# Kernel tuning notes

Measured on AMD Instinct MI355X. Metric: run time of the kernel, lower is better.

## Reference

```python
import jax, jax.numpy as jnp
import numpy as np

B, S, D_MODEL, H = 4, 2048, 1024, 16
DEPTH = D_MODEL // H  # 64


def setup_inputs() -> dict:
    key = jax.random.key(0)
    ks = jax.random.split(key, 12)
    inp = {
        "v": jax.random.normal(ks[0], (B, S, D_MODEL), jnp.float32),
        "k": jax.random.normal(ks[1], (B, S, D_MODEL), jnp.float32),
        "q": jax.random.normal(ks[2], (B, S, D_MODEL), jnp.float32),
        "mask": jnp.zeros((B, 1, 1, S), jnp.int32),  # unused by the layer
        # Dense(d_model) params (glorot-ish scale)
        "wq": jax.random.normal(ks[3], (D_MODEL, D_MODEL), jnp.float32) / np.sqrt(D_MODEL),
        "bq": jnp.zeros((D_MODEL,), jnp.float32),
        "wk": jax.random.normal(ks[4], (D_MODEL, D_MODEL), jnp.float32) / np.sqrt(D_MODEL),
        "bk": jnp.zeros((D_MODEL,), jnp.float32),
        "wv": jax.random.normal(ks[5], (D_MODEL, D_MODEL), jnp.float32) / np.sqrt(D_MODEL),
        "bv": jnp.zeros((D_MODEL,), jnp.float32),
        # global attention weights: [max_seq_len, 1], stddev=0.1
        "gqw": 0.1 * jax.random.normal(ks[6], (S, 1), jnp.float32),
        "gkw": 0.1 * jax.random.normal(ks[7], (S, 1), jnp.float32),
        "wo": jax.random.normal(ks[8], (D_MODEL, D_MODEL), jnp.float32) / np.sqrt(D_MODEL),
        "bo": jnp.zeros((D_MODEL,), jnp.float32),
    }
    return inp


def _split_heads(x):
    # [B, S, D] -> [B, H, S, depth]
    Bc = x.shape[0]
    return x.reshape(Bc, -1, H, DEPTH).transpose(0, 2, 1, 3)


def reference(v, k, q, mask, wq, bq, wk, bk, wv, bv, gqw, gkw, wo, bo):
    # QKV projections
    qh = _split_heads(q @ wq + bq)  # [B, H, S, depth]
    kh = _split_heads(k @ wk + bk)
    vh = _split_heads(v @ wv + bv)
    # Fastformer additive attention: mul -> seq-sum -> mul -> seq-sum -> mul -> add
    qh = qh * gqw                          # gqw [S,1] broadcasts over [B,H,S,depth]
    gq = jnp.sum(qh, axis=2, keepdims=True)  # global query [B,H,1,depth]
    kh = kh * gq * gkw
    gk = jnp.sum(kh, axis=2, keepdims=True)  # global key [B,H,1,depth]
    out = vh * gk + qh                       # [B,H,S,depth]
    # merge heads and output projection
    out = out.transpose(0, 2, 1, 3).reshape(out.shape[0], -1, D_MODEL)
    return out @ wo + bo
```

## Files before the change

kernel.cpp:

```cpp
#include <hip/hip_runtime.h>

#define DM 1024
#define BATCH 4
#define SEQ 2048
#define M_TOT (BATCH*SEQ)

typedef unsigned short ushort_t;
typedef __bf16 bf16x8 __attribute__((ext_vector_type(8)));
typedef float f32x4 __attribute__((ext_vector_type(4)));
typedef unsigned short u16x4 __attribute__((ext_vector_type(4)));
typedef unsigned short u16x8 __attribute__((ext_vector_type(8)));

__device__ __forceinline__ ushort_t f2bf(float f) {
  unsigned u = __builtin_bit_cast(unsigned, f);
  u = (u + 0x7fffu + ((u >> 16) & 1u)) >> 16;
  return (ushort_t)u;
}
__device__ __forceinline__ float bf2f(ushort_t h) {
  unsigned u = ((unsigned)h) << 16;
  return __builtin_bit_cast(float, u);
}

#define GLL(gp, lp)                                                            \
  __builtin_amdgcn_global_load_lds(                                            \
      (const __attribute__((address_space(1))) unsigned int*)(const void*)(gp),\
      (__attribute__((address_space(3))) unsigned int*)(void*)(lp), 16, 0, 0)

__device__ __forceinline__ size_t src_off(int row0, int e) {
  return (size_t)(row0 + (e >> 2)) * DM + (((e & 3) ^ ((e >> 3) & 3)) * 8);
}

__global__ void k_reduce(const float* __restrict__ q, const float* __restrict__ k,
                         const float* __restrict__ v,
                         const float* __restrict__ gqw, const float* __restrict__ gkw,
                         float* __restrict__ pq, float* __restrict__ pk,
                         float* __restrict__ G,
                         ushort_t* __restrict__ qb, ushort_t* __restrict__ vb) {
  const int b = blockIdx.x, sc = blockIdx.y;
  const int d0 = threadIdx.x * 4;
  const int s0 = sc * 8;
  const size_t base = ((size_t)b * SEQ + s0) * DM + d0;
  float aq0 = 0.f, aq1 = 0.f, aq2 = 0.f, aq3 = 0.f;
  float ak0 = 0.f, ak1 = 0.f, ak2 = 0.f, ak3 = 0.f;
  float sgq = 0.f, sgk = 0.f;
#pragma unroll
  for (int i = 0; i < 8; ++i) {
    const float wq_ = gqw[s0 + i], wk_ = gkw[s0 + i];
    const size_t off = base + (size_t)i * DM;
    const float4 qv = *(const float4*)(q + off);
    const float4 kv = *(const float4*)(k + off);
    const float4 vv = *(const float4*)(v + off);
    aq0 += wq_ * qv.x; aq1 += wq_ * qv.y; aq2 += wq_ * qv.z; aq3 += wq_ * qv.w;
    ak0 += wk_ * kv.x; ak1 += wk_ * kv.y; ak2 += wk_ * kv.z; ak3 += wk_ * kv.w;
    u16x4 oq, ov;
    oq[0] = f2bf(wq_ * qv.x); oq[1] = f2bf(wq_ * qv.y);
    oq[2] = f2bf(wq_ * qv.z); oq[3] = f2bf(wq_ * qv.w);
    ov[0] = f2bf(vv.x); ov[1] = f2bf(vv.y); ov[2] = f2bf(vv.z); ov[3] = f2bf(vv.w);
    *(u16x4*)(qb + off) = oq;
    *(u16x4*)(vb + off) = ov;
    sgq += wq_; sgk += wk_;
  }
  const size_t po = ((size_t)(sc * BATCH + b) << 10) + d0;
  *(float4*)(pq + po) = make_float4(aq0, aq1, aq2, aq3);
  *(float4*)(pk + po) = make_float4(ak0, ak1, ak2, ak3);
  if (b == 0 && threadIdx.x == 0) {
    atomicAdd(&G[0], sgq);
    atomicAdd(&G[1], sgk);
  }
}

__global__ void k_rsum(const float* __restrict__ pq, const float* __restrict__ pk,
                       float* __restrict__ qr, float* __restrict__ kr) {
  const int b = blockIdx.x;
  const int d = blockIdx.y * 256 + threadIdx.x;
  const int sg = blockIdx.z;
  float aq = 0.f, ak = 0.f;
#pragma unroll 4
  for (int s = sg * 32; s < sg * 32 + 32; ++s) {
    const size_t po = ((size_t)(s * BATCH + b) << 10) + d;
    aq += pq[po];
    ak += pk[po];
  }
  atomicAdd(&qr[b * DM + d], aq);
  atomicAdd(&kr[b * DM + d], ak);
}

__global__ void k_gpart(const float* __restrict__ wq, const float* __restrict__ wk,
                        const float* __restrict__ qr, const float* __restrict__ kr,
                        float* __restrict__ qacc, float* __restrict__ kacc) {
  const int d = blockIdx.x * 256 + threadIdx.x;
  const int k0 = blockIdx.y * 32;
  __shared__ float sq[4][32], sk[4][32];
  if (threadIdx.x < 128) {
    const int b = threadIdx.x >> 5, kk = threadIdx.x & 31;
    sq[b][kk] = qr[b * DM + k0 + kk];
    sk[b][kk] = kr[b * DM + k0 + kk];
  }
  __syncthreads();
  float aq[4] = {0.f, 0.f, 0.f, 0.f}, ak[4] = {0.f, 0.f, 0.f, 0.f};
#pragma unroll 8
  for (int kk = 0; kk < 32; ++kk) {
    const float wqv = wq[(size_t)(k0 + kk) * DM + d];
    const float wkv = wk[(size_t)(k0 + kk) * DM + d];
#pragma unroll
    for (int b = 0; b < 4; ++b) {
      aq[b] += sq[b][kk] * wqv;
      ak[b] += sk[b][kk] * wkv;
    }
  }
#pragma unroll
  for (int b = 0; b < 4; ++b) {
    atomicAdd(&qacc[b * DM + d], aq[b]);
    atomicAdd(&kacc[b * DM + d], ak[b]);
  }
}

__global__ void k_gfin(const float* __restrict__ qacc, const float* __restrict__ kacc,
                       const float* __restrict__ bq, const float* __restrict__ bk,
                       const float* __restrict__ G, float* __restrict__ gk) {
  const int i = blockIdx.x * 256 + threadIdx.x;
  const int d = i & (DM - 1);
  const float gqv = qacc[i] + bq[d] * G[0];
  const float gkr = kacc[i] + bk[d] * G[1];
  gk[i] = gqv * gkr;
}

__global__ void k_conv(const float* __restrict__ x0, ushort_t* __restrict__ y0,
                       const float* __restrict__ x1, ushort_t* __restrict__ y1) {
  const float* x = blockIdx.y ? x1 : x0;
  ushort_t* y = blockIdx.y ? y1 : y0;
  size_t i = (size_t)blockIdx.x * 256 + threadIdx.x;
  const float4* p = (const float4*)x + i * 2;
  float4 a = p[0], b = p[1];
  u16x8 o;
  o[0] = f2bf(a.x); o[1] = f2bf(a.y); o[2] = f2bf(a.z); o[3] = f2bf(a.w);
  o[4] = f2bf(b.x); o[5] = f2bf(b.y); o[6] = f2bf(b.z); o[7] = f2bf(b.w);
  *(u16x8*)(y + i * 8) = o;
}

__global__ void k_trans(const float* __restrict__ W, ushort_t* __restrict__ T) {
  __shared__ float ls[32][33];
  const int bi = blockIdx.x, bj = blockIdx.y;
#pragma unroll
  for (int p = 0; p < 4; ++p) {
    int e = threadIdx.x + p * 256;
    int r = e >> 5, c = e & 31;
    ls[r][c] = W[(size_t)(bi * 32 + r) * DM + bj * 32 + c];
  }
  __syncthreads();
#pragma unroll
  for (int p = 0; p < 4; ++p) {
    int e = threadIdx.x + p * 256;
    int r = e >> 5, c = e & 31;
    T[(size_t)(bj * 32 + r) * DM + bi * 32 + c] = f2bf(ls[c][r]);
  }
}

__global__ void k_wog(const ushort_t* __restrict__ woT, const float* __restrict__ gk,
                      ushort_t* __restrict__ wogT) {
  const size_t i = (size_t)blockIdx.x * 256 + threadIdx.x;
  const size_t c = i * 8;
  const int j0 = (int)(c & (DM - 1));
  const int b = (int)(c >> 20);
  u16x8 wv = *(const u16x8*)(woT + (c & ((1u << 20) - 1)));
  const float4 g0 = *(const float4*)(gk + b * DM + j0);
  const float4 g1 = *(const float4*)(gk + b * DM + j0 + 4);
  float g[8] = {g0.x, g0.y, g0.z, g0.w, g1.x, g1.y, g1.z, g1.w};
  u16x8 o;
#pragma unroll
  for (int j = 0; j < 8; ++j) o[j] = f2bf(bf2f(wv[j]) * g[j]);
  *(u16x8*)(wogT + i * 8) = o;
}

__global__ void k_bias(const float* __restrict__ wo, const float* __restrict__ bq,
                       const float* __restrict__ bv, const float* __restrict__ gk,
                       float* __restrict__ qbias, float* __restrict__ vbias) {
  const int n = blockIdx.x * 256 + threadIdx.x;
  const int k0 = blockIdx.y * 32;
  float aq = 0.f, av[4] = {0.f, 0.f, 0.f, 0.f};
  for (int kk = 0; kk < 32; ++kk) {
    const float w = wo[(size_t)(k0 + kk) * DM + n];
    aq += bq[k0 + kk] * w;
    const float bw = bv[k0 + kk] * w;
#pragma unroll
    for (int b = 0; b < 4; ++b) av[b] += bw * gk[b * DM + k0 + kk];
  }
  atomicAdd(&qbias[n], aq);
#pragma unroll
  for (int b = 0; b < 4; ++b) atomicAdd(&vbias[b * DM + n], av[b]);
}

__global__ void k_small(const ushort_t* __restrict__ woT, const ushort_t* __restrict__ wogT,
                        const ushort_t* __restrict__ wqB, const ushort_t* __restrict__ wvB,
                        ushort_t* __restrict__ WqoT, ushort_t* __restrict__ WvbT) {
  __shared__ __align__(16) ushort_t lsA[3][128 * 32];
  __shared__ __align__(16) ushort_t lsB[3][128 * 32];
  const int z = blockIdx.z;
  const ushort_t* A  = z == 0 ? woT : wogT + (size_t)(z - 1) * (DM * DM);
  const ushort_t* Bt = z == 0 ? wqB : wvB;
  ushort_t* Out      = z == 0 ? WqoT : WvbT + (size_t)(z - 1) * (DM * DM);

  const int tid = threadIdx.x;
  const int w = tid >> 6, lane = tid & 63;
  const int m0 = blockIdx.x * 128, n0 = blockIdx.y * 128;
  const int wr = w >> 1, wc = w & 1;
  const int c0 = w * 2, c1 = c0 + 1;
  const int e0 = c0 * 64 + lane, e1 = c1 * 64 + lane;
  const ushort_t* gA0 = A + src_off(m0, e0);
  const ushort_t* gA1 = A + src_off(m0, e1);
  const ushort_t* gB0 = Bt + src_off(n0, e0);
  const ushort_t* gB1 = Bt + src_off(n0, e1);

  int aoff[4], boff[4];
#pragma unroll
  for (int i = 0; i < 4; ++i) {
    const int ra = wr * 64 + i * 16 + (lane & 15);
    aoff[i] = ra * 32 + (((lane >> 4) ^ ((ra >> 1) & 3)) * 8);
    const int rb = wc * 64 + i * 16 + (lane & 15);
    boff[i] = rb * 32 + (((lane >> 4) ^ ((rb >> 1) & 3)) * 8);
  }

  f32x4 acc[4][4];
#pragma unroll
  for (int i = 0; i < 4; ++i)
#pragma unroll
    for (int j = 0; j < 4; ++j) acc[i][j] = (f32x4){0.f, 0.f, 0.f, 0.f};

  auto STAGE = [&](int tt, int buf) {
    const int o = tt * 32;
    GLL(gA0 + o, &lsA[buf][c0 * 512]);
    GLL(gA1 + o, &lsA[buf][c1 * 512]);
    GLL(gB0 + o, &lsB[buf][c0 * 512]);
    GLL(gB1 + o, &lsB[buf][c1 * 512]);
  };

  STAGE(0, 0);
  STAGE(1, 1);
#pragma unroll 1
  for (int t = 0; t < 32; ++t) {
    if (t < 31) { asm volatile("s_waitcnt vmcnt(4)" ::: "memory"); }
    else        { asm volatile("s_waitcnt vmcnt(0)" ::: "memory"); }
    __builtin_amdgcn_s_barrier();
    if (t + 2 < 32) STAGE(t + 2, (t + 2) % 3);
    const int cur = t % 3;
    bf16x8 av[4], bv[4];
#pragma unroll
    for (int i = 0; i < 4; ++i) av[i] = *(const bf16x8*)(&lsA[cur][aoff[i]]);
#pragma unroll
    for (int j = 0; j < 4; ++j) bv[j] = *(const bf16x8*)(&lsB[cur][boff[j]]);
#pragma unroll
    for (int i = 0; i < 4; ++i)
#pragma unroll
      for (int j = 0; j < 4; ++j)
        acc[i][j] = __builtin_amdgcn_mfma_f32_16x16x32_bf16(av[i], bv[j], acc[i][j], 0, 0, 0);
  }

  const int lr = (lane >> 4) * 4, lc = lane & 15;
  const int rbase = m0 + wr * 64, cbase = n0 + wc * 64;
#pragma unroll
  for (int j = 0; j < 4; ++j) {
    const int col = cbase + j * 16 + lc;
#pragma unroll
    for (int i = 0; i < 4; ++i)
#pragma unroll
      for (int t = 0; t < 4; ++t)
        Out[(size_t)(rbase + i * 16 + lr + t) * DM + col] = f2bf(acc[i][j][t]);
  }
}

__global__ __launch_bounds__(512, 1)
void k_big(const ushort_t* __restrict__ qb, const ushort_t* __restrict__ vb,
           const ushort_t* __restrict__ WqoT, const ushort_t* __restrict__ WvbT,
           const float* __restrict__ gqw, const float* __restrict__ qbias,
           const float* __restrict__ vbias, const float* __restrict__ bo,
           float* __restrict__ Out) {
  __shared__ __align__(16) ushort_t lsA[3][256 * 64];
  __shared__ __align__(16) ushort_t lsB[3][128 * 64];
  const int tid = threadIdx.x;
  const int w = tid >> 6, lane = tid & 63;
  const int m0 = blockIdx.x * 256, n0 = blockIdx.y * 128;
  const int b = m0 >> 11;
  const int wr = w >> 2, wc = w & 3;

  const int subrow = lane >> 3;
  const int srcslot = (lane & 7) ^ subrow;
  size_t offA[4], offB[2];
#pragma unroll
  for (int p = 0; p < 4; ++p) {
    const int row = (4 * w + p) * 8 + subrow;
    offA[p] = (size_t)(m0 + row) * DM + srcslot * 8;
  }
#pragma unroll
  for (int p = 0; p < 2; ++p) {
    const int row = (2 * w + p) * 8 + subrow;
    offB[p] = (size_t)(n0 + row) * DM + srcslot * 8;
  }
  const ushort_t* Bv = WvbT + (size_t)b * (DM * DM);

  const int g = lane >> 4, l7 = lane & 7, l15 = lane & 15;
  int aoff[2][8], boff[2][2];
#pragma unroll
  for (int kh = 0; kh < 2; ++kh) {
#pragma unroll
    for (int i = 0; i < 8; ++i) {
      const int ra = wr * 128 + i * 16 + l15;
      aoff[kh][i] = ra * 64 + (((kh * 4 + g) ^ l7) * 8);
    }
#pragma unroll
    for (int j = 0; j < 2; ++j) {
      const int rb = wc * 32 + j * 16 + l15;
      boff[kh][j] = rb * 64 + (((kh * 4 + g) ^ l7) * 8);
    }
  }

  f32x4 acc[8][2];
#pragma unroll
  for (int i = 0; i < 8; ++i)
#pragma unroll
    for (int j = 0; j < 2; ++j) acc[i][j] = (f32x4){0.f, 0.f, 0.f, 0.f};

  auto SRC = [&](int tt, const ushort_t*& Ab, const ushort_t*& Bb, int& k0) {
    if (tt < 16) { Ab = qb; Bb = WqoT; k0 = tt * 64; }
    else         { Ab = vb; Bb = Bv;   k0 = (tt - 16) * 64; }
  };
  auto STAGE_H0 = [&](int tt, int buf) {
    const ushort_t *Ab, *Bb; int k0; SRC(tt, Ab, Bb, k0);
    GLL(Ab + offA[0] + k0, &lsA[buf][(4 * w + 0) * 512]);
    GLL(Ab + offA[1] + k0, &lsA[buf][(4 * w + 1) * 512]);
    GLL(Bb + offB[0] + k0, &lsB[buf][(2 * w + 0) * 512]);
  };
  auto STAGE_H1 = [&](int tt, int buf) {
    const ushort_t *Ab, *Bb; int k0; SRC(tt, Ab, Bb, k0);
    GLL(Ab + offA[2] + k0, &lsA[buf][(4 * w + 2) * 512]);
    GLL(Ab + offA[3] + k0, &lsA[buf][(4 * w + 3) * 512]);
    GLL(Bb + offB[1] + k0, &lsB[buf][(2 * w + 1) * 512]);
  };

  STAGE_H0(0, 0); STAGE_H1(0, 0);
  STAGE_H0(1, 1); STAGE_H1(1, 1);
#pragma unroll 1
  for (int t = 0; t < 32; ++t) {
    const int cur = t % 3, nb = (t + 2) % 3;
    const bool st = (t + 2 < 32);
    if (t < 31) { asm volatile("s_waitcnt vmcnt(6)\n\ts_barrier" ::: "memory"); }
    else        { asm volatile("s_waitcnt vmcnt(0)\n\ts_barrier" ::: "memory"); }
    {
      bf16x8 av[8], bv[2];
#pragma unroll
      for (int i = 0; i < 8; ++i) av[i] = *(const bf16x8*)(&lsA[cur][aoff[0][i]]);
#pragma unroll
      for (int j = 0; j < 2; ++j) bv[j] = *(const bf16x8*)(&lsB[cur][boff[0][j]]);
      if (st) STAGE_H0(t + 2, nb);
      __builtin_amdgcn_s_setprio(1);
#pragma unroll
      for (int i = 0; i < 8; ++i)
#pragma unroll
        for (int j = 0; j < 2; ++j)
          acc[i][j] = __builtin_amdgcn_mfma_f32_16x16x32_bf16(av[i], bv[j], acc[i][j], 0, 0, 0);
      __builtin_amdgcn_s_setprio(0);
      asm volatile("s_barrier" ::: "memory");
    }
    {
      bf16x8 av[8], bv[2];
#pragma unroll
      for (int i = 0; i < 8; ++i) av[i] = *(const bf16x8*)(&lsA[cur][aoff[1][i]]);
#pragma unroll
      for (int j = 0; j < 2; ++j) bv[j] = *(const bf16x8*)(&lsB[cur][boff[1][j]]);
      if (st) STAGE_H1(t + 2, nb);
      __builtin_amdgcn_s_setprio(1);
#pragma unroll
      for (int i = 0; i < 8; ++i)
#pragma unroll
        for (int j = 0; j < 2; ++j)
          acc[i][j] = __builtin_amdgcn_mfma_f32_16x16x32_bf16(av[i], bv[j], acc[i][j], 0, 0, 0);
      __builtin_amdgcn_s_setprio(0);
      asm volatile("s_barrier" ::: "memory");
    }
  }

  const int lr = (lane >> 4) * 4, lc = lane & 15;
  const int rbase = m0 + wr * 128, cbase = n0 + wc * 32;
#pragma unroll
  for (int j = 0; j < 2; ++j) {
    const int col = cbase + j * 16 + lc;
    const float qbn = qbias[col];
    const float cb = vbias[b * DM + col] + bo[col];
#pragma unroll
    for (int i = 0; i < 8; ++i)
#pragma unroll
      for (int r = 0; r < 4; ++r) {
        const int row = rbase + i * 16 + lr + r;
        Out[(size_t)row * DM + col] = acc[i][j][r] + gqw[row & (SEQ - 1)] * qbn + cb;
      }
  }
}

extern "C" void kernel_launch(void* const* d_in, const int* in_sizes, int n_in,
                              void* d_out, int out_size, void* d_ws, size_t ws_size,
                              hipStream_t stream) {
  const float* v   = (const float*)d_in[0];
  const float* k   = (const float*)d_in[1];
  const float* q   = (const float*)d_in[2];
  const float* wq  = (const float*)d_in[4];
  const float* bq  = (const float*)d_in[5];
  const float* wk  = (const float*)d_in[6];
  const float* bk  = (const float*)d_in[7];
  const float* wv  = (const float*)d_in[8];
  const float* bv  = (const float*)d_in[9];
  const float* gqw = (const float*)d_in[10];
  const float* gkw = (const float*)d_in[11];
  const float* wo  = (const float*)d_in[12];
  const float* bo  = (const float*)d_in[13];
  float* out = (float*)d_out;
  float* wsf = (float*)d_ws;

  float* qr    = wsf + 0;
  float* kr    = wsf + 4096;
  float* qacc  = wsf + 8192;
  float* kacc  = wsf + 12288;
  float* G     = wsf + 16384;
  float* qbias = wsf + 16640;
  float* vbias = wsf + 17664;
  float* gk    = wsf + 21760;
  ushort_t* b16  = (ushort_t*)((char*)d_ws + (1 << 17));
  ushort_t* qb   = b16;
  ushort_t* vb   = qb + (size_t)M_TOT * DM;
  ushort_t* wqB  = vb + (size_t)M_TOT * DM;
  ushort_t* wvB  = wqB + (size_t)DM * DM;
  ushort_t* woT  = wvB + (size_t)DM * DM;
  ushort_t* WqoT = woT + (size_t)DM * DM;
  ushort_t* WvbT = WqoT + (size_t)DM * DM;
  ushort_t* wogT = (ushort_t*)out;
  float* pq = out + (1 << 22);
  float* pk = pq + (1 << 20);

  hipMemsetAsync(d_ws, 0, 21760 * sizeof(float), stream);

  k_conv<<<dim3((DM * DM / 8) / 256, 2), 256, 0, stream>>>(wq, wqB, wv, wvB);
  k_trans<<<dim3(32, 32), 256, 0, stream>>>(wo, woT);

  k_reduce<<<dim3(BATCH, SEQ / 8), 256, 0, stream>>>(q, k, v, gqw, gkw, pq, pk, G, qb, vb);
  k_rsum<<<dim3(BATCH, DM / 256, 8), 256, 0, stream>>>(pq, pk, qr, kr);

  k_gpart<<<dim3(DM / 256, DM / 32), 256, 0, stream>>>(wq, wk, qr, kr, qacc, kacc);
  k_gfin<<<(BATCH * DM) / 256, 256, 0, stream>>>(qacc, kacc, bq, bk, G, gk);

  k_wog<<<(BATCH * DM * DM / 8) / 256, 256, 0, stream>>>(woT, gk, wogT);
  k_bias<<<dim3(DM / 256, DM / 32), 256, 0, stream>>>(wo, bq, bv, gk, qbias, vbias);

  k_small<<<dim3(8, 8, 5), 256, 0, stream>>>(woT, wogT, wqB, wvB, WqoT, WvbT);

  k_big<<<dim3(M_TOT / 256, DM / 128), 512, 0, stream>>>(
      qb, vb, WqoT, WvbT, gqw, qbias, vbias, bo, out);
}
```

Baseline: 127.5 us.

## Software-pipeline LDS fragment reads across MFMA halves and template GEMM for weight fold

The big GEMM loop is restructured so each half-tile's LDS fragment reads are issued before the previous half's MFMAs. This double-buffers register fragments and drops one barrier per half-step, so LDS latency hides behind matrix math. The separate small weight-product GEMM is replaced by a templated instance of the same pipelined kernel (256x128 tiles, 512 threads, fewer blocks). The cost is higher register pressure from the doubled fragments, and lower parallelism for the small GEMM with only 160 blocks.

Result: faster. 123.1 us (-3.4%).

```diff
diff --git a/kernel.cpp b/kernel.cpp
--- a/kernel.cpp
+++ b/kernel.cpp
@@ -25,10 +25,6 @@
   __builtin_amdgcn_global_load_lds(                                            \
       (const __attribute__((address_space(1))) unsigned int*)(const void*)(gp),\
       (__attribute__((address_space(3))) unsigned int*)(void*)(lp), 16, 0, 0)
-
-__device__ __forceinline__ size_t src_off(int row0, int e) {
-  return (size_t)(row0 + (e >> 2)) * DM + (((e & 3) ^ ((e >> 3) & 3)) * 8);
-}
 
 __global__ void k_reduce(const float* __restrict__ q, const float* __restrict__ k,
                          const float* __restrict__ v,
@@ -190,97 +186,29 @@
   for (int b = 0; b < 4; ++b) atomicAdd(&vbias[b * DM + n], av[b]);
 }
 
-__global__ void k_small(const ushort_t* __restrict__ woT, const ushort_t* __restrict__ wogT,
-                        const ushort_t* __restrict__ wqB, const ushort_t* __restrict__ wvB,
-                        ushort_t* __restrict__ WqoT, ushort_t* __restrict__ WvbT) {
-  __shared__ __align__(16) ushort_t lsA[3][128 * 32];
-  __shared__ __align__(16) ushort_t lsB[3][128 * 32];
-  const int z = blockIdx.z;
-  const ushort_t* A  = z == 0 ? woT : wogT + (size_t)(z - 1) * (DM * DM);
-  const ushort_t* Bt = z == 0 ? wqB : wvB;
-  ushort_t* Out      = z == 0 ? WqoT : WvbT + (size_t)(z - 1) * (DM * DM);
-
-  const int tid = threadIdx.x;
-  const int w = tid >> 6, lane = tid & 63;
-  const int m0 = blockIdx.x * 128, n0 = blockIdx.y * 128;
-  const int wr = w >> 1, wc = w & 1;
-  const int c0 = w * 2, c1 = c0 + 1;
-  const int e0 = c0 * 64 + lane, e1 = c1 * 64 + lane;
-  const ushort_t* gA0 = A + src_off(m0, e0);
-  const ushort_t* gA1 = A + src_off(m0, e1);
-  const ushort_t* gB0 = Bt + src_off(n0, e0);
-  const ushort_t* gB1 = Bt + src_off(n0, e1);
-
-  int aoff[4], boff[4];
-#pragma unroll
-  for (int i = 0; i < 4; ++i) {
-    const int ra = wr * 64 + i * 16 + (lane & 15);
-    aoff[i] = ra * 32 + (((lane >> 4) ^ ((ra >> 1) & 3)) * 8);
-    const int rb = wc * 64 + i * 16 + (lane & 15);
-    boff[i] = rb * 32 + (((lane >> 4) ^ ((rb >> 1) & 3)) * 8);
-  }
-
-  f32x4 acc[4][4];
-#pragma unroll
-  for (int i = 0; i < 4; ++i)
-#pragma unroll
-    for (int j = 0; j < 4; ++j) acc[i][j] = (f32x4){0.f, 0.f, 0.f, 0.f};
-
-  auto STAGE = [&](int tt, int buf) {
-    const int o = tt * 32;
-    GLL(gA0 + o, &lsA[buf][c0 * 512]);
-    GLL(gA1 + o, &lsA[buf][c1 * 512]);
-    GLL(gB0 + o, &lsB[buf][c0 * 512]);
-    GLL(gB1 + o, &lsB[buf][c1 * 512]);
-  };
-
-  STAGE(0, 0);
-  STAGE(1, 1);
-#pragma unroll 1
-  for (int t = 0; t < 32; ++t) {
-    if (t < 31) { asm volatile("s_waitcnt vmcnt(4)" ::: "memory"); }
-    else        { asm volatile("s_waitcnt vmcnt(0)" ::: "memory"); }
-    __builtin_amdgcn_s_barrier();
-    if (t + 2 < 32) STAGE(t + 2, (t + 2) % 3);
-    const int cur = t % 3;
-    bf16x8 av[4], bv[4];
-#pragma unroll
-    for (int i = 0; i < 4; ++i) av[i] = *(const bf16x8*)(&lsA[cur][aoff[i]]);
-#pragma unroll
-    for (int j = 0; j < 4; ++j) bv[j] = *(const bf16x8*)(&lsB[cur][boff[j]]);
-#pragma unroll
-    for (int i = 0; i < 4; ++i)
-#pragma unroll
-      for (int j = 0; j < 4; ++j)
-        acc[i][j] = __builtin_amdgcn_mfma_f32_16x16x32_bf16(av[i], bv[j], acc[i][j], 0, 0, 0);
-  }
-
-  const int lr = (lane >> 4) * 4, lc = lane & 15;
-  const int rbase = m0 + wr * 64, cbase = n0 + wc * 64;
-#pragma unroll
-  for (int j = 0; j < 4; ++j) {
-    const int col = cbase + j * 16 + lc;
-#pragma unroll
-    for (int i = 0; i < 4; ++i)
-#pragma unroll
-      for (int t = 0; t < 4; ++t)
-        Out[(size_t)(rbase + i * 16 + lr + t) * DM + col] = f2bf(acc[i][j][t]);
-  }
-}
-
+template <int MODE, int NT>
 __global__ __launch_bounds__(512, 1)
-void k_big(const ushort_t* __restrict__ qb, const ushort_t* __restrict__ vb,
-           const ushort_t* __restrict__ WqoT, const ushort_t* __restrict__ WvbT,
-           const float* __restrict__ gqw, const float* __restrict__ qbias,
-           const float* __restrict__ vbias, const float* __restrict__ bo,
-           float* __restrict__ Out) {
+void k_pipe(const ushort_t* __restrict__ A0, const ushort_t* __restrict__ B0,
+            const ushort_t* __restrict__ A1, const ushort_t* __restrict__ B1,
+            const float* __restrict__ gqw, const float* __restrict__ qbias,
+            const float* __restrict__ vbias, const float* __restrict__ bo,
+            void* __restrict__ OutV) {
   __shared__ __align__(16) ushort_t lsA[3][256 * 64];
   __shared__ __align__(16) ushort_t lsB[3][128 * 64];
   const int tid = threadIdx.x;
   const int w = tid >> 6, lane = tid & 63;
   const int m0 = blockIdx.x * 256, n0 = blockIdx.y * 128;
-  const int b = m0 >> 11;
+  const int b = (MODE == 0) ? (m0 >> 11) : 0;
   const int wr = w >> 2, wc = w & 3;
+
+  const ushort_t *Aq, *Bq, *Av = nullptr, *Bv = nullptr;
+  if constexpr (MODE == 0) {
+    Aq = A0; Bq = B0; Av = A1; Bv = B1 + (size_t)b * (DM * DM);
+  } else {
+    const int z = blockIdx.z;
+    Aq = z ? A1 + (size_t)(z - 1) * (DM * DM) : A0;
+    Bq = z ? B1 : B0;
+  }
 
   const int subrow = lane >> 3;
   const int srcslot = (lane & 7) ^ subrow;
@@ -295,7 +223,6 @@
     const int row = (2 * w + p) * 8 + subrow;
     offB[p] = (size_t)(n0 + row) * DM + srcslot * 8;
   }
-  const ushort_t* Bv = WvbT + (size_t)b * (DM * DM);
 
   const int g = lane >> 4, l7 = lane & 7, l15 = lane & 15;
   int aoff[2][8], boff[2][2];
@@ -320,8 +247,8 @@
     for (int j = 0; j < 2; ++j) acc[i][j] = (f32x4){0.f, 0.f, 0.f, 0.f};
 
   auto SRC = [&](int tt, const ushort_t*& Ab, const ushort_t*& Bb, int& k0) {
-    if (tt < 16) { Ab = qb; Bb = WqoT; k0 = tt * 64; }
-    else         { Ab = vb; Bb = Bv;   k0 = (tt - 16) * 64; }
+    if (MODE == 0 && tt >= NT / 2) { Ab = Av; Bb = Bv; k0 = (tt - NT / 2) * 64; }
+    else                           { Ab = Aq; Bb = Bq; k0 = tt * 64; }
   };
   auto STAGE_H0 = [&](int tt, int buf) {
     const ushort_t *Ab, *Bb; int k0; SRC(tt, Ab, Bb, k0);
@@ -335,63 +262,75 @@
     GLL(Ab + offA[3] + k0, &lsA[buf][(4 * w + 3) * 512]);
     GLL(Bb + offB[1] + k0, &lsB[buf][(2 * w + 1) * 512]);
   };
+  auto READF = [&](bf16x8 (&av)[8], bf16x8 (&bv)[2], int cur, int kh) {
+#pragma unroll
+    for (int i = 0; i < 8; ++i) av[i] = *(const bf16x8*)(&lsA[cur][aoff[kh][i]]);
+#pragma unroll
+    for (int j = 0; j < 2; ++j) bv[j] = *(const bf16x8*)(&lsB[cur][boff[kh][j]]);
+  };
+  auto DOMFMA = [&](bf16x8 (&av)[8], bf16x8 (&bv)[2]) {
+    __builtin_amdgcn_s_setprio(1);
+#pragma unroll
+    for (int i = 0; i < 8; ++i)
+#pragma unroll
+      for (int j = 0; j < 2; ++j)
+        acc[i][j] = __builtin_amdgcn_mfma_f32_16x16x32_bf16(av[i], bv[j], acc[i][j], 0, 0, 0);
+    __builtin_amdgcn_s_setprio(0);
+  };
+
+  bf16x8 avA[8], bvA[2], avB[8], bvB[2];
 
   STAGE_H0(0, 0); STAGE_H1(0, 0);
   STAGE_H0(1, 1); STAGE_H1(1, 1);
+  asm volatile("s_waitcnt vmcnt(6)" ::: "memory");
+  __builtin_amdgcn_s_barrier();
+  READF(avA, bvA, 0, 0);
+
 #pragma unroll 1
-  for (int t = 0; t < 32; ++t) {
-    const int cur = t % 3, nb = (t + 2) % 3;
-    const bool st = (t + 2 < 32);
-    if (t < 31) { asm volatile("s_waitcnt vmcnt(6)\n\ts_barrier" ::: "memory"); }
-    else        { asm volatile("s_waitcnt vmcnt(0)\n\ts_barrier" ::: "memory"); }
-    {
-      bf16x8 av[8], bv[2];
-#pragma unroll
-      for (int i = 0; i < 8; ++i) av[i] = *(const bf16x8*)(&lsA[cur][aoff[0][i]]);
-#pragma unroll
-      for (int j = 0; j < 2; ++j) bv[j] = *(const bf16x8*)(&lsB[cur][boff[0][j]]);
-      if (st) STAGE_H0(t + 2, nb);
-      __builtin_amdgcn_s_setprio(1);
-#pragma unroll
-      for (int i = 0; i < 8; ++i)
-#pragma unroll
-        for (int j = 0; j < 2; ++j)
-          acc[i][j] = __builtin_amdgcn_mfma_f32_16x16x32_bf16(av[i], bv[j], acc[i][j], 0, 0, 0);
-      __builtin_amdgcn_s_setprio(0);
-      asm volatile("s_barrier" ::: "memory");
-    }
-    {
-      bf16x8 av[8], bv[2];
-#pragma unroll
-      for (int i = 0; i < 8; ++i) av[i] = *(const bf16x8*)(&lsA[cur][aoff[1][i]]);
-#pragma unroll
-      for (int j = 0; j < 2; ++j) bv[j] = *(const bf16x8*)(&lsB[cur][boff[1][j]]);
-      if (st) STAGE_H1(t + 2, nb);
-      __builtin_amdgcn_s_setprio(1);
-#pragma unroll
-      for (int i = 0; i < 8; ++i)
-#pragma unroll
-        for (int j = 0; j < 2; ++j)
-          acc[i][j] = __builtin_amdgcn_mfma_f32_16x16x32_bf16(av[i], bv[j], acc[i][j], 0, 0, 0);
-      __builtin_amdgcn_s_setprio(0);
-      asm volatile("s_barrier" ::: "memory");
-    }
+  for (int t = 0; t < NT; ++t) {
+    const int cur = t % 3, nb = (t + 2) % 3, nxt = (t + 1) % 3;
+    READF(avB, bvB, cur, 1);
+    if (t + 2 < NT) STAGE_H0(t + 2, nb);
+    DOMFMA(avA, bvA);
+    if (t + 1 < NT) {
+      if (t + 2 < NT) { asm volatile("s_waitcnt vmcnt(3)\n\ts_barrier" ::: "memory"); }
+      else            { asm volatile("s_waitcnt vmcnt(0)\n\ts_barrier" ::: "memory"); }
+      READF(avA, bvA, nxt, 0);
+      if (t + 2 < NT) STAGE_H1(t + 2, nb);
+    }
+    DOMFMA(avB, bvB);
   }
 
   const int lr = (lane >> 4) * 4, lc = lane & 15;
   const int rbase = m0 + wr * 128, cbase = n0 + wc * 32;
-#pragma unroll
-  for (int j = 0; j < 2; ++j) {
-    const int col = cbase + j * 16 + lc;
-    const float qbn = qbias[col];
-    const float cb = vbias[b * DM + col] + bo[col];
-#pragma unroll
-    for (int i = 0; i < 8; ++i)
-#pragma unroll
-      for (int r = 0; r < 4; ++r) {
-        const int row = rbase + i * 16 + lr + r;
-        Out[(size_t)row * DM + col] = acc[i][j][r] + gqw[row & (SEQ - 1)] * qbn + cb;
-      }
+  if constexpr (MODE == 0) {
+    float* Out = (float*)OutV;
+#pragma unroll
+    for (int j = 0; j < 2; ++j) {
+      const int col = cbase + j * 16 + lc;
+      const float qbn = qbias[col];
+      const float cb = vbias[b * DM + col] + bo[col];
+#pragma unroll
+      for (int i = 0; i < 8; ++i)
+#pragma unroll
+        for (int r = 0; r < 4; ++r) {
+          const int row = rbase + i * 16 + lr + r;
+          Out[(size_t)row * DM + col] = acc[i][j][r] + gqw[row & (SEQ - 1)] * qbn + cb;
+        }
+    }
+  } else {
+    ushort_t* Out = (ushort_t*)OutV + (size_t)blockIdx.z * (DM * DM);
+#pragma unroll
+    for (int j = 0; j < 2; ++j) {
+      const int col = cbase + j * 16 + lc;
+#pragma unroll
+      for (int i = 0; i < 8; ++i)
+#pragma unroll
+        for (int r = 0; r < 4; ++r) {
+          const int row = rbase + i * 16 + lr + r;
+          Out[(size_t)row * DM + col] = f2bf(acc[i][j][r]);
+        }
+    }
   }
 }
 
@@ -448,8 +387,9 @@
   k_wog<<<(BATCH * DM * DM / 8) / 256, 256, 0, stream>>>(woT, gk, wogT);
   k_bias<<<dim3(DM / 256, DM / 32), 256, 0, stream>>>(wo, bq, bv, gk, qbias, vbias);
 
-  k_small<<<dim3(8, 8, 5), 256, 0, stream>>>(woT, wogT, wqB, wvB, WqoT, WvbT);
-
-  k_big<<<dim3(M_TOT / 256, DM / 128), 512, 0, stream>>>(
-      qb, vb, WqoT, WvbT, gqw, qbias, vbias, bo, out);
-}
+  k_pipe<1, 16><<<dim3(4, 8, 5), 512, 0, stream>>>(
+      woT, wqB, wogT, wvB, nullptr, nullptr, nullptr, nullptr, WqoT);
+
+  k_pipe<0, 32><<<dim3(M_TOT / 256, DM / 128), 512, 0, stream>>>(
+      qb, WqoT, vb, WvbT, gqw, qbias, vbias, bo, out);
+}
```
